# Kernel tuning notes

Measured on AMD Instinct MI355X. Metric: run time of the kernel, lower is better.

## Reference

```python
import jax, jax.numpy as jnp
import numpy as np

NEG = 1.0e12  # large subtractive penalty from the original code


def setup_inputs() -> dict:
    key = jax.random.key(0)
    k1, k2, k3, k4 = jax.random.split(key, 4)
    b, q_len, ns, ls, e = 8, 512, 64, 128, 256
    q = jax.random.normal(k1, (b, q_len, e), dtype=jnp.float32)
    k = jax.random.normal(k2, (b, ns, ls, e), dtype=jnp.float32)
    v = jax.random.normal(k3, (b, ns, ls, e), dtype=jnp.float32)
    mask = jax.random.randint(k4, (b, ns, ls), 0, 2) > 0  # bool, True = keep
    return {"q": q, "k": k, "v": v, "mask": mask}


def reference(q, k, v, mask):
    # scores: (b, q_len, num_snippet, len_snippet)
    attn = jnp.einsum("bqe,bsle->bqsl", q, k)
    # original: attn = attn - (~mask) * 1e12, broadcast over q_len
    penalty = jnp.where(mask, 0.0, NEG).astype(attn.dtype)  # (b, s, l)
    attn = attn - penalty[:, None, :, :]
    attn = jax.nn.softmax(attn, axis=3)  # softmax within each snippet
    # weighted sum over len_snippet -> (b, q_len, num_snippet, e_dim)
    out = jnp.einsum("bqsl,bsle->bqse", attn, v)
    return out
```

## Files before the change

kernel.cpp:

```cpp
#include <hip/hip_runtime.h>

typedef _Float16 half8  __attribute__((ext_vector_type(8)));
typedef float    f32x4  __attribute__((ext_vector_type(4)));
typedef unsigned int u32;

#define QLEN  512
#define NS    64
#define LS    128
#define EDIM  256

__device__ __forceinline__ void block_sync_lds() {
    asm volatile("s_waitcnt lgkmcnt(0)" ::: "memory");
    __builtin_amdgcn_s_barrier();
    asm volatile("" ::: "memory");
}

__device__ __forceinline__ half8 cvt8(f32x4 a, f32x4 b) {
    half8 h;
    h[0]=(_Float16)a[0]; h[1]=(_Float16)a[1]; h[2]=(_Float16)a[2]; h[3]=(_Float16)a[3];
    h[4]=(_Float16)b[0]; h[5]=(_Float16)b[1]; h[6]=(_Float16)b[2]; h[7]=(_Float16)b[3];
    return h;
}

#define KLOAD(dst, lt) do {                                                   \
  _Pragma("unroll") for (int it = 0; it < 4; ++it) {                          \
    int f = it * 2048 + tid * 8; int r = f >> 8; int e0 = f & 255;            \
    const float* src = kbase + (size_t)((lt) * 32 + r) * EDIM + e0;           \
    dst[2*it]   = *(const f32x4*)src;                                         \
    dst[2*it+1] = *(const f32x4*)(src + 4); } } while (0)

#define KSTORE(sv, bi) do {                                                   \
  _Pragma("unroll") for (int it = 0; it < 4; ++it) {                          \
    int f = it * 2048 + tid * 8; int r = f >> 8; int e0 = f & 255;            \
    half8 h = cvt8(sv[2*it], sv[2*it+1]);                                     \
    *(half8*)(kvbuf + (bi) * 16384 + r * 512 + ((e0 * 2) ^ ((r & 7) << 4))) = h; } } while (0)

#define VLOAD(dL, dH, lt) do {                                                \
  const float* vb0 = vbase + (size_t)((lt) * 32 + vlh * 16) * EDIM + vp;      \
  _Pragma("unroll") for (int i = 0; i < 16; ++i) {                            \
    dL[i] = vb0[(size_t)i * EDIM];                                            \
    dH[i] = vb0[(size_t)i * EDIM + 128]; } } while (0)

#define VSTORE(dL, dH, p) do {                                                \
  _Pragma("unroll") for (int jj = 0; jj < 2; ++jj) {                          \
    half8 h0, h1;                                                             \
    _Pragma("unroll") for (int j = 0; j < 8; ++j) {                           \
      h0[j] = (_Float16)dL[jj*8+j]; h1[j] = (_Float16)dH[jj*8+j]; }           \
    int u   = vlh * 2 + jj;                                                   \
    int a0  = ((p) & 1) * 16384 + vp * 64 + ((u ^ ((vp >> 1) & 3)) * 16);     \
    *(half8*)(kvbuf + a0)        = h0;                                        \
    *(half8*)(kvbuf + a0 + 8192) = h1; } } while (0)

#define PV(lt) do {                                                           \
  u32 zx = sel2 ? pk0[2*(lt)+1] : pk0[2*(lt)];                                \
  u32 zy = sel2 ? pk1[2*(lt)+1] : pk1[2*(lt)];                                \
  u32 wx = sel2 ? pk0[2*(lt)]   : pk0[2*(lt)+1];                              \
  u32 wy = sel2 ? pk1[2*(lt)]   : pk1[2*(lt)+1];                              \
  u32 az0 = (u32)__shfl((int)zx, s0l, 64), az1 = (u32)__shfl((int)zy, s0l, 64); \
  u32 aw0 = (u32)__shfl((int)wx, s0l, 64), aw1 = (u32)__shfl((int)wy, s0l, 64); \
  u32 bz0 = (u32)__shfl((int)zx, s1l, 64), bz1 = (u32)__shfl((int)zy, s1l, 64); \
  u32 bw0 = (u32)__shfl((int)wx, s1l, 64), bw1 = (u32)__shfl((int)wy, s1l, 64); \
  union { u32 u[4]; half8 h; } pf;                                            \
  pf.u[0] = useZ ? az0 : aw0;  pf.u[1] = useZ ? az1 : aw1;                    \
  pf.u[2] = useZ ? bz0 : bw0;  pf.u[3] = useZ ? bz1 : bw1;                    \
  const unsigned char* vb = kvbuf + ((lt) & 1) * 16384;                       \
  __builtin_amdgcn_s_setprio(1);                                              \
  _Pragma("unroll") for (int et = 0; et < 16; ++et) {                         \
    int e = et * 16 + c;                                                      \
    half8 vf = *(const half8*)(vb + (size_t)e * 64 + ((g ^ ((c >> 1) & 3)) * 16)); \
    oacc[et] = __builtin_amdgcn_mfma_f32_16x16x32_f16(vf, pf.h, oacc[et], 0, 0, 0); } \
  __builtin_amdgcn_s_setprio(0); } while (0)

__global__ __launch_bounds__(256, 3)
void DotAttn_20083267076209_kernel(const float* __restrict__ qg,
                                   const float* __restrict__ kg,
                                   const float* __restrict__ vg,
                                   const int*   __restrict__ maskg,
                                   float*       __restrict__ outg)
{
    __shared__ __align__(16) unsigned char kvbuf[32768];

    const int tid  = threadIdx.x;
    const int lane = tid & 63;
    const int c    = lane & 15;
    const int g    = lane >> 4;
    const int vp   = tid & 127;
    const int vlh  = tid >> 7;
    const int w    = tid >> 6;

    const bool sel2 = (g >= 2);
    const bool useZ = (g == 0) || (g == 3);
    const int  s0l  = c + ((g & 1) << 5);
    const int  s1l  = s0l + 16;

    const int bid = blockIdx.x;
    const int xcd = bid & 7;
    const int qt  = (bid >> 3) & 7;
    const int b   = (bid >> 6) & 7;
    const int s   = (bid >> 9) * 8 + xcd;

    const float* kbase = kg + (size_t)(b * NS + s) * LS * EDIM;
    const float* vbase = vg + (size_t)(b * NS + s) * LS * EDIM;
    const float* qbase = qg + ((size_t)b * QLEN + (size_t)qt * 64 + (size_t)w * 16) * EDIM;

    const int* mb = maskg + (b * NS + s) * LS;
    int mraw0 = mb[lane];
    int mraw1 = mb[64 + lane];

    f32x4 kr0[8], kr1[8];
    KLOAD(kr0, 0);
    KLOAD(kr1, 1);

    half8 qf[8];
#pragma unroll
    for (int ks = 0; ks < 8; ++ks) {
        const float* p = qbase + (size_t)c * EDIM + ks * 32 + g * 8;
        qf[ks] = cvt8(*(const f32x4*)p, *(const f32x4*)(p + 4));
    }

    unsigned long long m0 = __ballot(mraw0 != 0);
    unsigned long long m1 = __ballot(mraw1 != 0);

    float vr0L[16], vr0H[16], vr1L[16], vr1H[16];

    f32x4 sacc[8];
#pragma unroll
    for (int t = 0; t < 8; ++t) sacc[t] = (f32x4){0.f, 0.f, 0.f, 0.f};

#pragma unroll
    for (int lt = 0; lt < 4; ++lt) {
        if ((lt & 1) == 0) KSTORE(kr0, 0); else KSTORE(kr1, 1);
        if (lt == 0) KLOAD(kr0, 2);
        else if (lt == 1) KLOAD(kr1, 3);
        else if (lt == 2) VLOAD(vr0L, vr0H, 0);
        else              VLOAD(vr1L, vr1H, 1);
        block_sync_lds();
        const unsigned char* kb = kvbuf + (lt & 1) * 16384;
        __builtin_amdgcn_s_setprio(1);
#pragma unroll
        for (int lb = 0; lb < 2; ++lb) {
            int row  = lb * 16 + c;
            int base = row * 512;
            int sw   = (c & 7) << 4;
#pragma unroll
            for (int ks = 0; ks < 8; ++ks) {
                half8 kf = *(const half8*)(kb + base + ((ks * 64 + g * 16) ^ sw));
                sacc[lt * 2 + lb] =
                    __builtin_amdgcn_mfma_f32_16x16x32_f16(kf, qf[ks], sacc[lt * 2 + lb], 0, 0, 0);
            }
        }
        __builtin_amdgcn_s_setprio(0);
    }

#pragma unroll
    for (int t = 0; t < 8; ++t) {
        unsigned bits = (unsigned)(((t < 4 ? m0 : m1) >> ((t & 3) * 16 + 4 * g)) & 0xFull);
#pragma unroll
        for (int r = 0; r < 4; ++r)
            if (!((bits >> r) & 1)) sacc[t][r] = -1e30f;
    }

    {
        float m = sacc[0][0];
#pragma unroll
        for (int t = 0; t < 8; ++t)
#pragma unroll
            for (int r = 0; r < 4; ++r) m = fmaxf(m, sacc[t][r]);
        m = fmaxf(m, __shfl_xor(m, 16, 64));
        m = fmaxf(m, __shfl_xor(m, 32, 64));
        float sum = 0.f;
#pragma unroll
        for (int t = 0; t < 8; ++t)
#pragma unroll
            for (int r = 0; r < 4; ++r) {
                float p = __expf(sacc[t][r] - m);
                sacc[t][r] = p;
                sum += p;
            }
        sum += __shfl_xor(sum, 16, 64);
        sum += __shfl_xor(sum, 32, 64);
        float inv = 1.f / sum;
#pragma unroll
        for (int t = 0; t < 8; ++t)
#pragma unroll
            for (int r = 0; r < 4; ++r) sacc[t][r] *= inv;
    }

    u32 pk0[8], pk1[8];
#pragma unroll
    for (int t = 0; t < 8; ++t) {
        pk0[t] = __builtin_bit_cast(u32, __builtin_amdgcn_cvt_pkrtz(sacc[t][0], sacc[t][1]));
        pk1[t] = __builtin_bit_cast(u32, __builtin_amdgcn_cvt_pkrtz(sacc[t][2], sacc[t][3]));
    }

    f32x4 oacc[16];
#pragma unroll
    for (int et = 0; et < 16; ++et) oacc[et] = (f32x4){0.f, 0.f, 0.f, 0.f};

    VSTORE(vr0L, vr0H, 0);
    VLOAD(vr0L, vr0H, 2);
    block_sync_lds();
    PV(0);
    VSTORE(vr1L, vr1H, 1);
    VLOAD(vr1L, vr1H, 3);
    block_sync_lds();
    PV(1);
    VSTORE(vr0L, vr0H, 2);
    block_sync_lds();
    PV(2);
    VSTORE(vr1L, vr1H, 3);
    block_sync_lds();
    PV(3);

    float* ob = outg + (((size_t)b * QLEN + (size_t)qt * 64 + w * 16 + c) * NS + s) * EDIM + 4 * g;
#pragma unroll
    for (int et = 0; et < 16; ++et)
        *(f32x4*)(ob + et * 16) = oacc[et];
}

extern "C" void kernel_launch(void* const* d_in, const int* in_sizes, int n_in,
                              void* d_out, int out_size, void* d_ws, size_t ws_size,
                              hipStream_t stream) {
    const float* q    = (const float*)d_in[0];
    const float* k    = (const float*)d_in[1];
    const float* v    = (const float*)d_in[2];
    const int*   mask = (const int*)d_in[3];
    float* out = (float*)d_out;
    dim3 grid(4096);
    dim3 block(256);
    hipLaunchKernelGGL(DotAttn_20083267076209_kernel, grid, block, 0, stream,
                       q, k, v, mask, out);
}
```

Baseline: 166.0 us.

## Split fused attention into separate score/softmax and PV kernels via output scratch

Splits the single fused kernel into two launches. The first computes QK scores and softmax and writes fp16 probabilities into the output buffer as scratch. The second reads those probabilities back and does the PV MFMA pass. This cuts register pressure in the score kernel (occupancy hint raised to 4) and removes the cross-lane shuffles that rearranged probabilities into MFMA operand layout. The cost is an extra launch, an extra global write and read of the probabilities, and serialisation between the phases.

New measurement: 212.0 us. 27.7% more time.

```diff
diff --git a/kernel.cpp b/kernel.cpp
--- a/kernel.cpp
+++ b/kernel.cpp
@@ -48,35 +48,30 @@
       h0[j] = (_Float16)dL[jj*8+j]; h1[j] = (_Float16)dH[jj*8+j]; }           \
     int u   = vlh * 2 + jj;                                                   \
     int a0  = ((p) & 1) * 16384 + vp * 64 + ((u ^ ((vp >> 1) & 3)) * 16);     \
-    *(half8*)(kvbuf + a0)        = h0;                                        \
-    *(half8*)(kvbuf + a0 + 8192) = h1; } } while (0)
+    *(half8*)(vbuf + a0)        = h0;                                         \
+    *(half8*)(vbuf + a0 + 8192) = h1; } } while (0)
 
 #define PV(lt) do {                                                           \
-  u32 zx = sel2 ? pk0[2*(lt)+1] : pk0[2*(lt)];                                \
-  u32 zy = sel2 ? pk1[2*(lt)+1] : pk1[2*(lt)];                                \
-  u32 wx = sel2 ? pk0[2*(lt)]   : pk0[2*(lt)+1];                              \
-  u32 wy = sel2 ? pk1[2*(lt)]   : pk1[2*(lt)+1];                              \
-  u32 az0 = (u32)__shfl((int)zx, s0l, 64), az1 = (u32)__shfl((int)zy, s0l, 64); \
-  u32 aw0 = (u32)__shfl((int)wx, s0l, 64), aw1 = (u32)__shfl((int)wy, s0l, 64); \
-  u32 bz0 = (u32)__shfl((int)zx, s1l, 64), bz1 = (u32)__shfl((int)zy, s1l, 64); \
-  u32 bw0 = (u32)__shfl((int)wx, s1l, 64), bw1 = (u32)__shfl((int)wy, s1l, 64); \
-  union { u32 u[4]; half8 h; } pf;                                            \
-  pf.u[0] = useZ ? az0 : aw0;  pf.u[1] = useZ ? az1 : aw1;                    \
-  pf.u[2] = useZ ? bz0 : bw0;  pf.u[3] = useZ ? bz1 : bw1;                    \
-  const unsigned char* vb = kvbuf + ((lt) & 1) * 16384;                       \
+  const unsigned char* vb = vbuf + ((lt) & 1) * 16384;                        \
   __builtin_amdgcn_s_setprio(1);                                              \
   _Pragma("unroll") for (int et = 0; et < 16; ++et) {                         \
     int e = et * 16 + c;                                                      \
     half8 vf = *(const half8*)(vb + (size_t)e * 64 + ((g ^ ((c >> 1) & 3)) * 16)); \
-    oacc[et] = __builtin_amdgcn_mfma_f32_16x16x32_f16(vf, pf.h, oacc[et], 0, 0, 0); } \
+    oacc[et] = __builtin_amdgcn_mfma_f32_16x16x32_f16(vf, pf[lt], oacc[et], 0, 0, 0); } \
   __builtin_amdgcn_s_setprio(0); } while (0)
 
-__global__ __launch_bounds__(256, 3)
-void DotAttn_20083267076209_kernel(const float* __restrict__ qg,
-                                   const float* __restrict__ kg,
-                                   const float* __restrict__ vg,
-                                   const int*   __restrict__ maskg,
-                                   float*       __restrict__ outg)
+#define DECODE()                                                              \
+    const int bid = blockIdx.x;                                               \
+    const int xcd = bid & 7;                                                  \
+    const int qt  = (bid >> 3) & 7;                                           \
+    const int b   = (bid >> 6) & 7;                                           \
+    const int s   = (bid >> 9) * 8 + xcd;
+
+__global__ __launch_bounds__(256, 4)
+void dotattn_s_kernel(const float* __restrict__ qg,
+                      const float* __restrict__ kg,
+                      const int*   __restrict__ maskg,
+                      float*       __restrict__ outg)
 {
     __shared__ __align__(16) unsigned char kvbuf[32768];
 
@@ -84,23 +79,11 @@
     const int lane = tid & 63;
     const int c    = lane & 15;
     const int g    = lane >> 4;
-    const int vp   = tid & 127;
-    const int vlh  = tid >> 7;
     const int w    = tid >> 6;
 
-    const bool sel2 = (g >= 2);
-    const bool useZ = (g == 0) || (g == 3);
-    const int  s0l  = c + ((g & 1) << 5);
-    const int  s1l  = s0l + 16;
-
-    const int bid = blockIdx.x;
-    const int xcd = bid & 7;
-    const int qt  = (bid >> 3) & 7;
-    const int b   = (bid >> 6) & 7;
-    const int s   = (bid >> 9) * 8 + xcd;
+    DECODE();
 
     const float* kbase = kg + (size_t)(b * NS + s) * LS * EDIM;
-    const float* vbase = vg + (size_t)(b * NS + s) * LS * EDIM;
     const float* qbase = qg + ((size_t)b * QLEN + (size_t)qt * 64 + (size_t)w * 16) * EDIM;
 
     const int* mb = maskg + (b * NS + s) * LS;
@@ -120,8 +103,6 @@
 
     unsigned long long m0 = __ballot(mraw0 != 0);
     unsigned long long m1 = __ballot(mraw1 != 0);
-
-    float vr0L[16], vr0H[16], vr1L[16], vr1H[16];
 
     f32x4 sacc[8];
 #pragma unroll
@@ -132,8 +113,6 @@
         if ((lt & 1) == 0) KSTORE(kr0, 0); else KSTORE(kr1, 1);
         if (lt == 0) KLOAD(kr0, 2);
         else if (lt == 1) KLOAD(kr1, 3);
-        else if (lt == 2) VLOAD(vr0L, vr0H, 0);
-        else              VLOAD(vr1L, vr1H, 1);
         block_sync_lds();
         const unsigned char* kb = kvbuf + (lt & 1) * 16384;
         __builtin_amdgcn_s_setprio(1);
@@ -150,6 +129,7 @@
             }
         }
         __builtin_amdgcn_s_setprio(0);
+        block_sync_lds();
     }
 
 #pragma unroll
@@ -186,12 +166,45 @@
             for (int r = 0; r < 4; ++r) sacc[t][r] *= inv;
     }
 
-    u32 pk0[8], pk1[8];
-#pragma unroll
-    for (int t = 0; t < 8; ++t) {
-        pk0[t] = __builtin_bit_cast(u32, __builtin_amdgcn_cvt_pkrtz(sacc[t][0], sacc[t][1]));
-        pk1[t] = __builtin_bit_cast(u32, __builtin_amdgcn_cvt_pkrtz(sacc[t][2], sacc[t][3]));
-    }
+    {
+        u32* pu = (u32*)(outg + (((size_t)b * QLEN + (size_t)qt * 64 + w * 16 + c) * NS + s) * EDIM);
+#pragma unroll
+        for (int t = 0; t < 8; ++t) {
+            uint2 pr;
+            pr.x = __builtin_bit_cast(u32, __builtin_amdgcn_cvt_pkrtz(sacc[t][0], sacc[t][1]));
+            pr.y = __builtin_bit_cast(u32, __builtin_amdgcn_cvt_pkrtz(sacc[t][2], sacc[t][3]));
+            *(uint2*)(pu + t * 8 + 2 * g) = pr;
+        }
+    }
+}
+
+__global__ __launch_bounds__(256, 3)
+void dotattn_pv_kernel(const float* __restrict__ vg,
+                       float*       __restrict__ outg)
+{
+    __shared__ __align__(16) unsigned char vbuf[32768];
+
+    const int tid  = threadIdx.x;
+    const int lane = tid & 63;
+    const int c    = lane & 15;
+    const int g    = lane >> 4;
+    const int vp   = tid & 127;
+    const int vlh  = tid >> 7;
+    const int w    = tid >> 6;
+
+    DECODE();
+
+    const float* vbase = vg + (size_t)(b * NS + s) * LS * EDIM;
+    float* orow = outg + (((size_t)b * QLEN + (size_t)qt * 64 + w * 16 + c) * NS + s) * EDIM;
+
+    half8 pf[4];
+#pragma unroll
+    for (int lt = 0; lt < 4; ++lt)
+        pf[lt] = *(const half8*)((const unsigned char*)orow + lt * 64 + g * 16);
+
+    float vr0L[16], vr0H[16], vr1L[16], vr1H[16];
+    VLOAD(vr0L, vr0H, 0);
+    VLOAD(vr1L, vr1H, 1);
 
     f32x4 oacc[16];
 #pragma unroll
@@ -212,7 +225,7 @@
     block_sync_lds();
     PV(3);
 
-    float* ob = outg + (((size_t)b * QLEN + (size_t)qt * 64 + w * 16 + c) * NS + s) * EDIM + 4 * g;
+    float* ob = orow + 4 * g;
 #pragma unroll
     for (int et = 0; et < 16; ++et)
         *(f32x4*)(ob + et * 16) = oacc[et];
@@ -228,6 +241,6 @@
     float* out = (float*)d_out;
     dim3 grid(4096);
     dim3 block(256);
-    hipLaunchKernelGGL(DotAttn_20083267076209_kernel, grid, block, 0, stream,
-                       q, k, v, mask, out);
-}
+    hipLaunchKernelGGL(dotattn_s_kernel,  grid, block, 0, stream, q, k, mask, out);
+    hipLaunchKernelGGL(dotattn_pv_kernel, grid, block, 0, stream, v, out);
+}
```
